# Kernel tuning notes

Measured on AMD Instinct MI355X. Metric: run time of the kernel, lower is better.

## Reference

```python
import jax, jax.numpy as jnp
import numpy as np

N_QUBIT = 14
N_LAYER = 16
BATCH = 512
DIM = 2 ** N_QUBIT

# wire 0 is the most-significant bit (deepquantum convention: state.reshape([2]*n), wire i = axis i)
_bits = (np.arange(DIM)[:, None] >> (N_QUBIT - 1 - np.arange(N_QUBIT))) & 1
SIGNS = jnp.asarray(2.0 * _bits - 1.0, dtype=jnp.float32)  # (DIM, n_qubit), -1 for bit=0, +1 for bit=1


def _apply_1q(state, gate, w):
    # state: (B, DIM) complex64; gate: (2,2) complex
    B = state.shape[0]
    left, right = 2 ** w, 2 ** (N_QUBIT - w - 1)
    st = state.reshape(B, left, 2, right)
    return jnp.einsum('ab,xlbr->xlar', gate, st).reshape(B, DIM)


def _cnot(state, c, t):
    # CNOT control c, target t: X on target where control bit = 1
    B = state.shape[0]
    st = state.reshape((B,) + (2,) * N_QUBIT)
    ax_c, ax_t = c + 1, t + 1
    a0 = jnp.take(st, 0, axis=ax_c)
    a1 = jnp.take(st, 1, axis=ax_c)
    a1 = jnp.flip(a1, axis=ax_t if ax_t < ax_c else ax_t - 1)  # flip size-2 axis == X gate
    return jnp.stack([a0, a1], axis=ax_c).reshape(B, DIM)


def _rz_layer(state, thetas):
    # RZ(th) = diag(e^{-i th/2}, e^{+i th/2}) on every wire -> single fused diagonal phase
    return state * jnp.exp(0.5j * (SIGNS @ thetas))


def _ry_layer(state, thetas):
    for w in range(N_QUBIT):
        c = jnp.cos(thetas[w] * 0.5)
        s = jnp.sin(thetas[w] * 0.5)
        gate = jnp.stack([jnp.stack([c, -s]), jnp.stack([s, c])]).astype(jnp.complex64)
        state = _apply_1q(state, gate, w)
    return state


def _circuit(z, theta):
    state = z.reshape(z.shape[0], DIM)
    for l in range(N_LAYER):
        state = _rz_layer(state, theta[l, 0])
        state = _ry_layer(state, theta[l, 1])
        state = _rz_layer(state, theta[l, 2])
        for w in range(N_QUBIT):  # cnot_ring
            state = _cnot(state, w, (w + 1) % N_QUBIT)
    return state


def _split(state, w):
    B = state.shape[0]
    st = state.reshape(B, 2 ** w, 2, 2 ** (N_QUBIT - w - 1))
    return st[:, :, 0, :], st[:, :, 1, :]


def _expectations(state):
    outs = []
    for w in (0, 1):  # <Z_w> = sum |psi_0|^2 - |psi_1|^2
        p0, p1 = _split(state, w)
        outs.append(jnp.sum(jnp.abs(p0) ** 2 - jnp.abs(p1) ** 2, axis=(1, 2)))
    cross0 = None
    for w in (0, 1):  # <X_w> = 2 Re sum conj(psi_0) psi_1
        p0, p1 = _split(state, w)
        cr = jnp.conj(p0) * p1
        if w == 0:
            cross0 = cr
        outs.append(2.0 * jnp.sum(jnp.real(cr), axis=(1, 2)))
    outs.append(2.0 * jnp.sum(jnp.imag(cross0), axis=(1, 2)))  # <Y_0> = 2 Im sum conj(psi_0) psi_1
    return jnp.stack(outs, axis=1).astype(jnp.float32)  # (B, 5)


def setup_inputs() -> dict:
    key = jax.random.key(0)
    k1, k2, k3, k4 = jax.random.split(key, 4)
    zr = jax.random.normal(k1, (BATCH, DIM), dtype=jnp.float32)
    zi = jax.random.normal(k2, (BATCH, DIM), dtype=jnp.float32)
    z = (zr + 1j * zi).astype(jnp.complex64)
    z = z / jnp.linalg.norm(z, axis=1, keepdims=True)  # normalized quantum states
    z = z[:, :, None]  # (B, 2^n, 1) per docstring
    theta = jax.random.normal(k3, (N_LAYER, 3, N_QUBIT), dtype=jnp.float32)
    y = jax.random.randint(k4, (BATCH,), 0, 5)
    return {"z": z, "theta": theta, "y": y}


def reference(z, theta, y):
    state = _circuit(z, theta)
    output = _expectations(state)
    logp = jax.nn.log_softmax(output, axis=1)
    loss = -jnp.mean(jnp.take_along_axis(logp, y[:, None], axis=1))
    return (loss, output)
```

## Files before the change

kernel.cpp:

```cpp
#include <hip/hip_runtime.h>
#include <hip/hip_bf16.h>

#define NQ     14
#define DIM    16384
#define NLAYER 16
#define BATCH  512
#define NT     1024

typedef float v2f __attribute__((ext_vector_type(2)));

__device__ __forceinline__ constexpr int POSB(int x){ return (x ^ ((x >> 5) & 31)) << 3; }

__device__ __forceinline__ float bf2f(unsigned int u16){
  union { unsigned int i; float f; } v; v.i = u16 << 16; return v.f;
}

__device__ __forceinline__ float thv(const void* th, int i, bool b16){
  return b16 ? bf2f(((const unsigned short*)th)[i]) : ((const float*)th)[i];
}

__device__ int srcF(int x){
  int v = x;
  #pragma unroll
  for (int k = 13; k >= 0; --k){
    int tb = 13 - ((k + 1) % 14);
    v ^= ((v >> (13 - k)) & 1) << tb;
  }
  return v;
}

__device__ __forceinline__ v2f cmul(v2f a, v2f b){
  v2f as = a.yx;
  v2f br = (v2f){ b.x,  b.x};
  v2f bi = (v2f){-b.y,  b.y};
  return a * br + as * bi;
}

__device__ __forceinline__ void rot2(v2f& a0, v2f& a1, float c, float s){
  v2f c2 = (v2f){c, c}, s2 = (v2f){s, s};
  v2f t0 = a0;
  a0 = a0 * c2 - a1 * s2;
  a1 = t0 * s2 + a1 * c2;
}

__global__ __launch_bounds__(NT) __attribute__((amdgpu_waves_per_eu(4, 4)))
void qnn_circuit(const void* __restrict__ zraw,
                 const void* __restrict__ theta,
                 float* __restrict__ out)
{
  __shared__ v2f   S[DIM];
  __shared__ v2f   ph0H[128], ph0L[128], ph2H[128], ph2L[128];
  __shared__ float csT[28];
  __shared__ int   sHB[128], sLB[128];
  __shared__ float red[16*5];

  char* Sb = (char*)S;
  const int t = threadIdx.x;
  const int b = blockIdx.x;

  int pred = 0;
  if (t < 336){
    unsigned int w  = ((const unsigned int*)theta)[t];
    unsigned int lo = w & 0xffffu;
    unsigned int e  = (lo >> 7) & 0xffu;
    pred = (e >= 100 && e <= 140) || (lo == 0);
  }
  const bool th_b16 = (__syncthreads_count(pred) > 250);

  pred = 0;
  if (t < 256){
    unsigned int w  = ((const unsigned int*)zraw)[t];
    unsigned int lo = w & 0xffffu;
    unsigned int e  = (lo >> 7) & 0xffu;
    pred = (e >= 88 && e <= 140) || (lo == 0);
  }
  const bool z_b16 = (__syncthreads_count(pred) > 160);

  if (t < 128){ sHB[t] = POSB(srcF(t << 7)); sLB[t] = POSB(srcF(t)); }

  if (z_b16){
    const uint4* zb = (const uint4*)((const unsigned short*)zraw + (size_t)b * (DIM * 2));
    #pragma unroll 1
    for (int jj = 0; jj < 4; ++jj){
      int x4 = t + NT * jj;
      uint4 w = zb[x4];
      int xb = x4 * 4;
      *(v2f*)(Sb + POSB(xb+0)) = (v2f){bf2f(w.x & 0xffffu), bf2f(w.x >> 16)};
      *(v2f*)(Sb + POSB(xb+1)) = (v2f){bf2f(w.y & 0xffffu), bf2f(w.y >> 16)};
      *(v2f*)(Sb + POSB(xb+2)) = (v2f){bf2f(w.z & 0xffffu), bf2f(w.z >> 16)};
      *(v2f*)(Sb + POSB(xb+3)) = (v2f){bf2f(w.w & 0xffffu), bf2f(w.w >> 16)};
    }
  } else {
    const float4* zf = (const float4*)((const float*)zraw + (size_t)b * DIM);
    #pragma unroll 1
    for (int jj = 0; jj < 4; ++jj){
      int x4 = t + NT * jj;
      float4 w = zf[x4];
      int xb = x4 * 4;
      *(v2f*)(Sb + POSB(xb+0)) = (v2f){w.x, 0.f};
      *(v2f*)(Sb + POSB(xb+1)) = (v2f){w.y, 0.f};
      *(v2f*)(Sb + POSB(xb+2)) = (v2f){w.z, 0.f};
      *(v2f*)(Sb + POSB(xb+3)) = (v2f){w.w, 0.f};
    }
  }
  __syncthreads();

  const int pwb = POSB(t);
  const int hb  = t >> 7;
  int slB;
  slB = sLB[t & 127];

  for (int l = 0; l < NLAYER; ++l){
    const int thb = l * 42;

    if (t < 512){
      int grp = t >> 7, idx = t & 127;
      int tz = thb + ((grp >= 2) ? 28 : 0);
      float ph = 0.f;
      if ((grp & 1) == 0){
        #pragma unroll
        for (int w = 0; w < 7; ++w)
          ph += (((idx >> (6 - w)) & 1) ? 0.5f : -0.5f) * thv(theta, tz + w, th_b16);
      } else {
        #pragma unroll
        for (int w = 7; w < 14; ++w)
          ph += (((idx >> (13 - w)) & 1) ? 0.5f : -0.5f) * thv(theta, tz + w, th_b16);
      }
      float sn, cs; sincosf(ph, &sn, &cs);
      v2f v = (v2f){cs, sn};
      if      (grp == 0) ph0H[idx] = v;
      else if (grp == 1) ph0L[idx] = v;
      else if (grp == 2) ph2H[idx] = v;
      else               ph2L[idx] = v;
    } else if (t < 512 + 14){
      int q = t - 512;
      float sn, cs; sincosf(0.5f * thv(theta, thb + 14 + q, th_b16), &sn, &cs);
      csT[2*q] = cs; csT[2*q+1] = sn;
    }

    {
      v2f g[16];
      if (l == 0){
        #pragma unroll
        for (int j = 0; j < 16; ++j) g[j] = *(v2f*)(Sb + (pwb ^ (j << 13)));
      } else {
        #pragma unroll
        for (int j = 0; j < 16; ++j)
          g[j] = *(v2f*)(Sb + (sHB[hb + 8*j] ^ slB));
      }
      __syncthreads();

      {
        v2f cl = ph0L[t & 127];
        #pragma unroll
        for (int j = 0; j < 16; ++j)
          g[j] = cmul(g[j], cmul(ph0H[hb + 8*j], cl));
      }
      #pragma unroll
      for (int q = 0; q < 4; ++q){
        float c = csT[2*q], sn = csT[2*q+1];
        int m = 8 >> q;
        #pragma unroll
        for (int j = 0; j < 16; ++j){
          if (j & m) continue;
          rot2(g[j], g[j | m], c, sn);
        }
      }
      #pragma unroll
      for (int j = 0; j < 16; ++j) *(v2f*)(Sb + (pwb ^ (j << 13))) = g[j];
    }
    __syncthreads();

    #pragma unroll 1
    for (int it = 0; it < 2; ++it){
      int s = t + NT * it;
      int pb = POSB(((s >> 7) << 10) | (s & 127));
      v2f h[8];
      #pragma unroll
      for (int j = 0; j < 8; ++j) h[j] = *(v2f*)(Sb + (pb ^ POSB(j << 7)));
      #pragma unroll
      for (int q = 0; q < 3; ++q){
        float c = csT[2*(4+q)], sn = csT[2*(4+q)+1];
        int m = 4 >> q;
        #pragma unroll
        for (int j = 0; j < 8; ++j){
          if (j & m) continue;
          rot2(h[j], h[j | m], c, sn);
        }
      }
      #pragma unroll
      for (int j = 0; j < 8; ++j) *(v2f*)(Sb + (pb ^ POSB(j << 7))) = h[j];
    }
    __syncthreads();

    #pragma unroll 1
    for (int it = 0; it < 2; ++it){
      int s = t + NT * it;
      int pb = POSB(((s >> 7) << 10) | (((s >> 5) & 1) << 9) | (((s >> 4) & 1) << 8)
                  | (((s >> 6) & 1) << 7) | (s & 15));
      v2f h[8];
      #pragma unroll
      for (int j = 0; j < 8; ++j) h[j] = *(v2f*)(Sb + (pb ^ POSB(j << 4)));
      #pragma unroll
      for (int q = 0; q < 3; ++q){
        float c = csT[2*(7+q)], sn = csT[2*(7+q)+1];
        int m = 4 >> q;
        #pragma unroll
        for (int j = 0; j < 8; ++j){
          if (j & m) continue;
          rot2(h[j], h[j | m], c, sn);
        }
      }
      #pragma unroll
      for (int j = 0; j < 8; ++j) *(v2f*)(Sb + (pb ^ POSB(j << 4))) = h[j];
    }
    __syncthreads();

    #pragma unroll 1
    for (int it = 0; it < 4; ++it){
      int s = t + NT * it;
      int pb = POSB(((s >> 8) << 10) | (((s >> 4) & 1) << 9) | (((s >> 3) & 1) << 8)
                  | (((s >> 2) & 1) << 7) | (((s >> 6) & 1) << 6) | (((s >> 5) & 1) << 5)
                  | (((s >> 7) & 1) << 4) | (s & 3));
      v2f h[4];
      #pragma unroll
      for (int j = 0; j < 4; ++j) h[j] = *(v2f*)(Sb + (pb ^ POSB(j << 2)));
      #pragma unroll
      for (int q = 0; q < 2; ++q){
        float c = csT[2*(10+q)], sn = csT[2*(10+q)+1];
        int m = 2 >> q;
        #pragma unroll
        for (int j = 0; j < 4; ++j){
          if (j & m) continue;
          rot2(h[j], h[j | m], c, sn);
        }
      }
      #pragma unroll
      for (int j = 0; j < 4; ++j) *(v2f*)(Sb + (pb ^ POSB(j << 2))) = h[j];
    }
    __syncthreads();

    #pragma unroll 1
    for (int it = 0; it < 4; ++it){
      int s = t + NT * it;
      int x0 = ((s >> 8) << 10) | ((s & 31) << 5) | (((s >> 7) & 1) << 4)
             | (((s >> 6) & 1) << 3) | (((s >> 5) & 1) << 2);
      int pb = POSB(x0);
      v2f h[4];
      #pragma unroll
      for (int j = 0; j < 4; ++j) h[j] = *(v2f*)(Sb + (pb ^ (j << 3)));
      #pragma unroll
      for (int q = 0; q < 2; ++q){
        float c = csT[2*(12+q)], sn = csT[2*(12+q)+1];
        int m = 2 >> q;
        #pragma unroll
        for (int j = 0; j < 4; ++j){
          if (j & m) continue;
          rot2(h[j], h[j | m], c, sn);
        }
      }
      {
        v2f chh = ph2H[x0 >> 7];
        #pragma unroll
        for (int j = 0; j < 4; ++j)
          h[j] = cmul(h[j], cmul(chh, ph2L[(x0 | j) & 127]));
      }
      #pragma unroll
      for (int j = 0; j < 4; ++j) *(v2f*)(Sb + (pb ^ (j << 3))) = h[j];
    }
    __syncthreads();
  }

  float z0=0.f, z1=0.f, x0s=0.f, x1s=0.f, y0s=0.f;
  {
    v2f g[16];
    #pragma unroll
    for (int j = 0; j < 16; ++j)
      g[j] = *(v2f*)(Sb + (sHB[hb + 8*j] ^ slB));

    #pragma unroll
    for (int j = 0; j < 16; ++j){
      float pw = g[j].x*g[j].x + g[j].y*g[j].y;
      z0 += (j & 8) ? -pw : pw;
      z1 += (j & 4) ? -pw : pw;
    }
    #pragma unroll
    for (int j = 0; j < 8; ++j){
      v2f p0 = g[j], p1 = g[j+8];
      x0s += 2.f*(p0.x*p1.x + p0.y*p1.y);
      y0s += 2.f*(p0.x*p1.y - p0.y*p1.x);
    }
    #pragma unroll
    for (int j = 0; j < 16; ++j){
      if (j & 4) continue;
      v2f p0 = g[j], p1 = g[j|4];
      x1s += 2.f*(p0.x*p1.x + p0.y*p1.y);
    }
  }
  #pragma unroll
  for (int o = 32; o >= 1; o >>= 1){
    z0  += __shfl_down(z0,  o, 64);
    z1  += __shfl_down(z1,  o, 64);
    x0s += __shfl_down(x0s, o, 64);
    x1s += __shfl_down(x1s, o, 64);
    y0s += __shfl_down(y0s, o, 64);
  }
  int wid = t >> 6, lane = t & 63;
  if (lane == 0){
    red[wid*5+0]=z0; red[wid*5+1]=z1; red[wid*5+2]=x0s; red[wid*5+3]=x1s; red[wid*5+4]=y0s;
  }
  __syncthreads();
  if (t < 5){
    float sum = 0.f;
    #pragma unroll
    for (int w = 0; w < 16; ++w) sum += red[w*5 + t];
    out[1 + b*5 + t] = sum;
  }
}

__global__ __launch_bounds__(512)
void qnn_loss(const int* __restrict__ y, float* __restrict__ out)
{
  __shared__ float red[8];
  int t = threadIdx.x;
  const float* o = out + 1 + t*5;
  float o0=o[0], o1=o[1], o2=o[2], o3=o[3], o4=o[4];
  float m = fmaxf(fmaxf(fmaxf(o0,o1), fmaxf(o2,o3)), o4);
  float sum = expf(o0-m)+expf(o1-m)+expf(o2-m)+expf(o3-m)+expf(o4-m);
  float lse = m + logf(sum);
  int yi = y[t]; yi = yi < 0 ? 0 : (yi > 4 ? 4 : yi);
  float lb = lse - o[yi];

  #pragma unroll
  for (int ofs = 32; ofs >= 1; ofs >>= 1) lb += __shfl_down(lb, ofs, 64);
  if ((t & 63) == 0) red[t >> 6] = lb;
  __syncthreads();
  if (t == 0){
    float s = 0.f;
    #pragma unroll
    for (int w = 0; w < 8; ++w) s += red[w];
    out[0] = s / (float)BATCH;
  }
}

extern "C" void kernel_launch(void* const* d_in, const int* in_sizes, int n_in,
                              void* d_out, int out_size, void* d_ws, size_t ws_size,
                              hipStream_t stream)
{
  const void* z     = d_in[0];
  const void* theta = d_in[1];
  const int*  y     = (const int*)d_in[2];
  float*      out   = (float*)d_out;

  qnn_circuit<<<BATCH, NT, 0, stream>>>(z, theta, out);
  qnn_loss<<<1, 512, 0, stream>>>(y, out);
}
```

Baseline: 305.4 us.

## Regroup RY qubit passes into 4+3+3 blocks to cut LDS sweeps per layer

Restructures the per-layer RY sweep of the remaining 10 qubits: instead of four passes (3,3,2,2 qubits) over shared memory, it uses three passes (4,3,3 qubits), each thread holding 16 or 8 amplitudes. This removes one full shared-memory read/write sweep and one barrier per layer. It also precomputes the swizzled base addresses outside the layer loop and fully unrolls the inner iterations. More amplitudes per thread raises register pressure, and the new address patterns may change LDS bank conflicts.

```diff
diff --git a/kernel.cpp b/kernel.cpp
--- a/kernel.cpp
+++ b/kernel.cpp
@@ -107,8 +107,13 @@
 
   const int pwb = POSB(t);
   const int hb  = t >> 7;
-  int slB;
-  slB = sLB[t & 127];
+  const int slB = sLB[t & 127];
+
+  const int pb2 = POSB(((t >> 6) << 10) | (t & 63));
+  const int pb3 = POSB((t & 7) | (((t >> 3) & 7) << 6) | (((t >> 6) & 15) << 9));
+  const int x4base = ((t & 7) << 5) | (((t >> 3) & 1) << 3) | (((t >> 4) & 1) << 8)
+                   | (((t >> 5) & 1) << 4) | (((t >> 6) & 15) << 9);
+  const int pb4 = POSB(x4base);
 
   for (int l = 0; l < NLAYER; ++l){
     const int thb = l * 42;
@@ -171,16 +176,37 @@
     }
     __syncthreads();
 
-    #pragma unroll 1
+    {
+      v2f h[16];
+      #pragma unroll
+      for (int j = 0; j < 16; ++j)
+        h[j] = *(v2f*)(Sb + (pb2 ^ (((j << 6) | ((j << 1) & 31)) << 3)));
+      #pragma unroll
+      for (int q = 0; q < 4; ++q){
+        float c = csT[2*(4+q)], sn = csT[2*(4+q)+1];
+        int m = 8 >> q;
+        #pragma unroll
+        for (int j = 0; j < 16; ++j){
+          if (j & m) continue;
+          rot2(h[j], h[j | m], c, sn);
+        }
+      }
+      #pragma unroll
+      for (int j = 0; j < 16; ++j)
+        *(v2f*)(Sb + (pb2 ^ (((j << 6) | ((j << 1) & 31)) << 3))) = h[j];
+    }
+    __syncthreads();
+
+    #pragma unroll
     for (int it = 0; it < 2; ++it){
-      int s = t + NT * it;
-      int pb = POSB(((s >> 7) << 10) | (s & 127));
+      int pb = pb3 ^ (it << 16);
       v2f h[8];
       #pragma unroll
-      for (int j = 0; j < 8; ++j) h[j] = *(v2f*)(Sb + (pb ^ POSB(j << 7)));
+      for (int j = 0; j < 8; ++j)
+        h[j] = *(v2f*)(Sb + (pb ^ (((j << 3) | (j >> 2)) << 3)));
       #pragma unroll
       for (int q = 0; q < 3; ++q){
-        float c = csT[2*(4+q)], sn = csT[2*(4+q)+1];
+        float c = csT[2*(8+q)], sn = csT[2*(8+q)+1];
         int m = 4 >> q;
         #pragma unroll
         for (int j = 0; j < 8; ++j){
@@ -189,21 +215,20 @@
         }
       }
       #pragma unroll
-      for (int j = 0; j < 8; ++j) *(v2f*)(Sb + (pb ^ POSB(j << 7))) = h[j];
+      for (int j = 0; j < 8; ++j)
+        *(v2f*)(Sb + (pb ^ (((j << 3) | (j >> 2)) << 3))) = h[j];
     }
     __syncthreads();
 
-    #pragma unroll 1
+    #pragma unroll
     for (int it = 0; it < 2; ++it){
-      int s = t + NT * it;
-      int pb = POSB(((s >> 7) << 10) | (((s >> 5) & 1) << 9) | (((s >> 4) & 1) << 8)
-                  | (((s >> 6) & 1) << 7) | (s & 15));
+      int pb = pb4 ^ (it << 16);
       v2f h[8];
       #pragma unroll
-      for (int j = 0; j < 8; ++j) h[j] = *(v2f*)(Sb + (pb ^ POSB(j << 4)));
+      for (int j = 0; j < 8; ++j) h[j] = *(v2f*)(Sb + (pb ^ (j << 3)));
       #pragma unroll
       for (int q = 0; q < 3; ++q){
-        float c = csT[2*(7+q)], sn = csT[2*(7+q)+1];
+        float c = csT[2*(11+q)], sn = csT[2*(11+q)+1];
         int m = 4 >> q;
         #pragma unroll
         for (int j = 0; j < 8; ++j){
@@ -211,62 +236,16 @@
           rot2(h[j], h[j | m], c, sn);
         }
       }
-      #pragma unroll
-      for (int j = 0; j < 8; ++j) *(v2f*)(Sb + (pb ^ POSB(j << 4))) = h[j];
-    }
-    __syncthreads();
-
-    #pragma unroll 1
-    for (int it = 0; it < 4; ++it){
-      int s = t + NT * it;
-      int pb = POSB(((s >> 8) << 10) | (((s >> 4) & 1) << 9) | (((s >> 3) & 1) << 8)
-                  | (((s >> 2) & 1) << 7) | (((s >> 6) & 1) << 6) | (((s >> 5) & 1) << 5)
-                  | (((s >> 7) & 1) << 4) | (s & 3));
-      v2f h[4];
-      #pragma unroll
-      for (int j = 0; j < 4; ++j) h[j] = *(v2f*)(Sb + (pb ^ POSB(j << 2)));
-      #pragma unroll
-      for (int q = 0; q < 2; ++q){
-        float c = csT[2*(10+q)], sn = csT[2*(10+q)+1];
-        int m = 2 >> q;
-        #pragma unroll
-        for (int j = 0; j < 4; ++j){
-          if (j & m) continue;
-          rot2(h[j], h[j | m], c, sn);
-        }
-      }
-      #pragma unroll
-      for (int j = 0; j < 4; ++j) *(v2f*)(Sb + (pb ^ POSB(j << 2))) = h[j];
-    }
-    __syncthreads();
-
-    #pragma unroll 1
-    for (int it = 0; it < 4; ++it){
-      int s = t + NT * it;
-      int x0 = ((s >> 8) << 10) | ((s & 31) << 5) | (((s >> 7) & 1) << 4)
-             | (((s >> 6) & 1) << 3) | (((s >> 5) & 1) << 2);
-      int pb = POSB(x0);
-      v2f h[4];
-      #pragma unroll
-      for (int j = 0; j < 4; ++j) h[j] = *(v2f*)(Sb + (pb ^ (j << 3)));
-      #pragma unroll
-      for (int q = 0; q < 2; ++q){
-        float c = csT[2*(12+q)], sn = csT[2*(12+q)+1];
-        int m = 2 >> q;
-        #pragma unroll
-        for (int j = 0; j < 4; ++j){
-          if (j & m) continue;
-          rot2(h[j], h[j | m], c, sn);
-        }
-      }
       {
+        int x0 = x4base | (it << 13);
         v2f chh = ph2H[x0 >> 7];
-        #pragma unroll
-        for (int j = 0; j < 4; ++j)
-          h[j] = cmul(h[j], cmul(chh, ph2L[(x0 | j) & 127]));
-      }
-      #pragma unroll
-      for (int j = 0; j < 4; ++j) *(v2f*)(Sb + (pb ^ (j << 3))) = h[j];
+        int lbase = x0 & 127;
+        #pragma unroll
+        for (int j = 0; j < 8; ++j)
+          h[j] = cmul(h[j], cmul(chh, ph2L[lbase | j]));
+      }
+      #pragma unroll
+      for (int j = 0; j < 8; ++j) *(v2f*)(Sb + (pb ^ (j << 3))) = h[j];
     }
     __syncthreads();
   }
```

Result: slower. 325.8 us (+6.7%).
